# Optimization experiments

Measured on AMD Instinct MI355X. Metric: run time of the kernel, lower is better.

Reference implementation:

```python
import jax, jax.numpy as jnp
import numpy as np

N_X_AXIS = 128
N_Y_AXIS = 128
X_RANGE = (-2.0, 2.0)
Y_RANGE = (-2.0, 2.0)
BATCH = 4
N_CTX = 1024


def make_grid():
    # Give_2d_Grid: flattened (n_x*n_y, 2) grid, x-major (consistent with
    # the view(batch, n_x_axis, n_y_axis, 3) reshape in forward).
    gx = jnp.linspace(X_RANGE[0], X_RANGE[1], N_X_AXIS, dtype=jnp.float32)
    gy = jnp.linspace(Y_RANGE[0], Y_RANGE[1], N_Y_AXIS, dtype=jnp.float32)
    xx, yy = jnp.meshgrid(gx, gy, indexing='ij')  # (n_x, n_y)
    return jnp.stack([xx.ravel(), yy.ravel()], axis=-1)  # (n_x*n_y, 2)


def setup_inputs() -> dict:
    key = jax.random.key(0)
    k1, k2 = jax.random.split(key)
    X = jax.random.normal(k1, (BATCH, N_CTX, 2), dtype=jnp.float32)
    Y = jax.random.normal(k2, (BATCH, N_CTX, 2), dtype=jnp.float32)
    grid = make_grid()
    return {"X": X, "Y": Y, "grid": grid}


def reference(X, Y, grid):
    # RBF Gram matrix between grid points and context points X.
    # k(a,b) = exp(-||a-b||^2 / (2 l^2)), l = 1 (default length scale).
    # d2: (B, G, n)
    d2 = jnp.sum((grid[None, :, None, :] - X[:, None, :, :]) ** 2, axis=-1)
    Gram = jnp.exp(-0.5 * d2)  # (B, G, n)

    # Psi: prepend a column of ones -> (B, n, 3)
    ones = jnp.ones(Y.shape[:2] + (1,), dtype=Y.dtype)
    Expand_Y = jnp.concatenate([ones, Y], axis=-1)

    # Feature map: (B, G, 3)
    FM = jnp.einsum('bgn,bnc->bgc', Gram, Expand_Y)

    # Density-normalize the value channels by the density channel.
    density = FM[..., 0:1]
    FM = jnp.concatenate([density, FM[..., 1:] / density], axis=-1)

    # (B, G, 3) -> (B, n_x, n_y, 3) -> (B, 3, n_y, n_x)
    out = FM.reshape(X.shape[0], N_X_AXIS, N_Y_AXIS, 3)
    return out.transpose(0, 3, 2, 1)
```

## Files before the change

### kernel.cpp

```cpp
#include <hip/hip_runtime.h>


#define N_CTX   1024
#define G_PER_B 16384
#define NQ      64
#define CHUNK   (N_CTX / NQ)
#define TPB     4
#define SSTRIDE (CHUNK + 1)

typedef float fv4 __attribute__((ext_vector_type(4)));

__device__ __forceinline__ float fast_exp2(float x) {
#if __has_builtin(__builtin_amdgcn_exp2f)
  return __builtin_amdgcn_exp2f(x);
#else
  return exp2f(x);
#endif
}

#define RED_BYTES (32 * TPB * 13 * 16)
#define S_BYTES   ((N_CTX + NQ) * 16)

__global__ __launch_bounds__(256, 4) void convcnp_encoder_kernel(
    const float* __restrict__ X,
    const float* __restrict__ Y,
    const float* __restrict__ grid,
    float* __restrict__ out)
{
  __shared__ __attribute__((aligned(16))) unsigned char smem[RED_BYTES];
  float4* s = (float4*)smem;
  fv4 (*red)[TPB][13] = (fv4 (*)[TPB][13])smem;

  const int t    = threadIdx.x;
  const int tile = t & (TPB - 1);
  const int q    = t >> 2;

  const int tau = blockIdx.x * TPB + tile;
  const int b   = tau >> 10;
  const int rem = tau & 1023;
  const int ixt = rem & 31;
  const int jyt = rem >> 5;

  const float SC = 0.84932180028801907f;

  const float2* Xb = (const float2*)(X + b * (N_CTX * 2));
  const float2* Yb = (const float2*)(Y + b * (N_CTX * 2));
#pragma unroll
  for (int k = 0; k < 4; ++k) {
    int n = t + 256 * k;
    float2 x = Xb[n];
    float2 y = Yb[n];
    s[n + (n >> 4)] = make_float4(x.x * SC, x.y * SC, y.x, y.y);
  }

  fv4 gxs;
#pragma unroll
  for (int a = 0; a < 4; ++a)
    gxs[a] = grid[(4 * ixt + a) * 256] * SC;
  float gys[4];
#pragma unroll
  for (int bb = 0; bb < 4; ++bb)
    gys[bb] = grid[2 * (4 * jyt + bb) + 1] * SC;

  __syncthreads();

  fv4 acc0[4], acc1[4], acc2[4];
#pragma unroll
  for (int bb = 0; bb < 4; ++bb) {
    acc0[bb] = (fv4){0.f, 0.f, 0.f, 0.f};
    acc1[bb] = (fv4){0.f, 0.f, 0.f, 0.f};
    acc2[bb] = (fv4){0.f, 0.f, 0.f, 0.f};
  }

  const float4* sp = &s[q * SSTRIDE];
#pragma unroll 4
  for (int it = 0; it < CHUNK; ++it) {
    float4 v = sp[it];
    fv4 dx = gxs - v.x;
    fv4 ex;
#pragma unroll
    for (int a = 0; a < 4; ++a) ex[a] = fast_exp2(-(dx[a] * dx[a]));
    float ey[4], ey0[4], ey1[4];
#pragma unroll
    for (int bb = 0; bb < 4; ++bb) {
      float dy = gys[bb] - v.y;
      float e  = fast_exp2(-(dy * dy));
      ey[bb]  = e;
      ey0[bb] = e * v.z;
      ey1[bb] = e * v.w;
    }
#pragma unroll
    for (int bb = 0; bb < 4; ++bb) {
      acc0[bb] += ex * ey[bb];
      acc1[bb] += ex * ey0[bb];
      acc2[bb] += ex * ey1[bb];
    }
  }

  __syncthreads();

#pragma unroll
  for (int step = 32; step >= 1; step >>= 1) {
    if (q >= step && q < 2 * step) {
      fv4* d = &red[q - step][tile][0];
#pragma unroll
      for (int bb = 0; bb < 4; ++bb) {
        d[bb] = acc0[bb]; d[4 + bb] = acc1[bb]; d[8 + bb] = acc2[bb];
      }
    }
    __syncthreads();
    if (q < step) {
      fv4* r = &red[q][tile][0];
#pragma unroll
      for (int bb = 0; bb < 4; ++bb) {
        acc0[bb] += r[bb]; acc1[bb] += r[4 + bb]; acc2[bb] += r[8 + bb];
      }
    }
    __syncthreads();
  }

  if (q == 0) {
    const int ob = b * (3 * G_PER_B) + jyt * 4 * 128 + ixt * 4;
#pragma unroll
    for (int bb = 0; bb < 4; ++bb) {
      fv4 d  = acc0[bb];
      fv4 o1 = acc1[bb] / d;
      fv4 o2 = acc2[bb] / d;
      const int row = ob + bb * 128;
      *(fv4*)(out + row)                = d;
      *(fv4*)(out + row + G_PER_B)      = o1;
      *(fv4*)(out + row + 2 * G_PER_B)  = o2;
    }
  }
}

extern "C" void kernel_launch(void* const* d_in, const int* in_sizes, int n_in,
                              void* d_out, int out_size, void* d_ws, size_t ws_size,
                              hipStream_t stream) {
  const float* X    = (const float*)d_in[0];
  const float* Y    = (const float*)d_in[1];
  const float* grid = (const float*)d_in[2];
  float* out        = (float*)d_out;

  convcnp_encoder_kernel<<<dim3(1024), dim3(256), 0, stream>>>(X, Y, grid, out);
}
```

Baseline: 71.66 us.

## Factor RBF kernel into separable exp tables and bf16 split-precision MFMA GEMM

Uses the separability of the Gaussian (exp of x-distance times exp of y-distance) to precompute per-axis exponential tables. It stores them as hi/lo bf16 pairs so that three bf16 products recover near-fp32 accuracy. The contraction over context points becomes a split-K MFMA GEMM across many blocks, followed by a finishing kernel that sums the partials and normalises by density. This removes most exp evaluations and the scalar FMA work, at the cost of two extra launches, workspace traffic for tables and partials, and some precision loss from the bf16 split.

After: 77.83 us. +8.6%, slower.

```diff
diff --git a/kernel.cpp b/kernel.cpp
--- a/kernel.cpp
+++ b/kernel.cpp
@@ -1,14 +1,13 @@
 #include <hip/hip_runtime.h>
 
 
-#define N_CTX   1024
-#define G_PER_B 16384
-#define NQ      64
-#define CHUNK   (N_CTX / NQ)
-#define TPB     4
-#define SSTRIDE (CHUNK + 1)
+#define N_CTXP  1024
+#define PL      524288
+#define TABB    (8 * PL * 2)
+#define KSL     24
 
-typedef float fv4 __attribute__((ext_vector_type(4)));
+typedef float  f32x4  __attribute__((ext_vector_type(4)));
+typedef short  bf16x8 __attribute__((ext_vector_type(8)));
 
 __device__ __forceinline__ float fast_exp2(float x) {
 #if __has_builtin(__builtin_amdgcn_exp2f)
@@ -18,120 +17,159 @@
 #endif
 }
 
-#define RED_BYTES (32 * TPB * 13 * 16)
-#define S_BYTES   ((N_CTX + NQ) * 16)
+__device__ __forceinline__ unsigned short f2bf(float v) {
+  unsigned u = __float_as_uint(v);
+  return (unsigned short)((u + 0x7fff + ((u >> 16) & 1)) >> 16);
+}
+__device__ __forceinline__ float bf2f(unsigned short h) {
+  return __uint_as_float(((unsigned)h) << 16);
+}
 
-__global__ __launch_bounds__(256, 4) void convcnp_encoder_kernel(
-    const float* __restrict__ X,
-    const float* __restrict__ Y,
-    const float* __restrict__ grid,
-    float* __restrict__ out)
+__global__ __launch_bounds__(256) void k1_tables(
+    const float* __restrict__ X, const float* __restrict__ Y,
+    const float* __restrict__ grid, unsigned short* __restrict__ tab)
 {
-  __shared__ __attribute__((aligned(16))) unsigned char smem[RED_BYTES];
-  float4* s = (float4*)smem;
-  fv4 (*red)[TPB][13] = (fv4 (*)[TPB][13])smem;
+  const float SC = 0.84932180028801907f;
+  const int tid  = blockIdx.x * 256 + threadIdx.x;
+  const int side = tid >> 16;
+  const int u    = tid & 65535;
+  const int b    = u >> 14;
+  const int i    = (u >> 7) & 127;
+  const int n0   = (u & 127) * 8;
+  const int base = (b * 128 + i) * 1024 + n0;
 
-  const int t    = threadIdx.x;
-  const int tile = t & (TPB - 1);
-  const int q    = t >> 2;
+  const float2* Xb = (const float2*)X + b * 1024 + n0;
+  if (side == 0) {
+    const float gx = grid[i * 256];
+    bf16x8 vh, vl;
+#pragma unroll
+    for (int j = 0; j < 8; ++j) {
+      float d = SC * (gx - Xb[j].x);
+      float e = fast_exp2(-(d * d));
+      unsigned short h = f2bf(e);
+      vh[j] = (short)h;
+      vl[j] = (short)f2bf(e - bf2f(h));
+    }
+    *(bf16x8*)(tab + 0 * PL + base) = vh;
+    *(bf16x8*)(tab + 1 * PL + base) = vl;
+  } else {
+    const float gy = grid[2 * i + 1];
+    const float2* Yb = (const float2*)Y + b * 1024 + n0;
+    bf16x8 eh, el, ah, al, bh, bl;
+#pragma unroll
+    for (int j = 0; j < 8; ++j) {
+      float d  = SC * (gy - Xb[j].y);
+      float e  = fast_exp2(-(d * d));
+      float v0 = e * Yb[j].x;
+      float v1 = e * Yb[j].y;
+      unsigned short h;
+      h = f2bf(e);  eh[j] = (short)h; el[j] = (short)f2bf(e  - bf2f(h));
+      h = f2bf(v0); ah[j] = (short)h; al[j] = (short)f2bf(v0 - bf2f(h));
+      h = f2bf(v1); bh[j] = (short)h; bl[j] = (short)f2bf(v1 - bf2f(h));
+    }
+    *(bf16x8*)(tab + 2 * PL + base) = eh;
+    *(bf16x8*)(tab + 3 * PL + base) = el;
+    *(bf16x8*)(tab + 4 * PL + base) = ah;
+    *(bf16x8*)(tab + 5 * PL + base) = al;
+    *(bf16x8*)(tab + 6 * PL + base) = bh;
+    *(bf16x8*)(tab + 7 * PL + base) = bl;
+  }
+}
 
-  const int tau = blockIdx.x * TPB + tile;
-  const int b   = tau >> 10;
-  const int rem = tau & 1023;
-  const int ixt = rem & 31;
-  const int jyt = rem >> 5;
+__global__ __launch_bounds__(256) void k2_gemm(
+    const unsigned short* __restrict__ tab, float* __restrict__ part)
+{
+  const int bid   = blockIdx.x;
+  const int ks    = bid % KSL;
+  const int r     = bid / KSL;
+  const int ixreg = r & 1, jyreg = (r >> 1) & 1, c = (r >> 2) % 3, b = r / 12;
+  const int sl    = ks >> 3;
+  const int n0    = (ks & 7) * 128;
+  const int Apl   = 2 + 2 * c + (sl == 2 ? 1 : 0);
+  const int Bpl   = (sl == 1) ? 1 : 0;
 
-  const float SC = 0.84932180028801907f;
+  __shared__ unsigned short Alds[64 * 128];
+  __shared__ unsigned short Blds[64 * 128];
 
-  const float2* Xb = (const float2*)(X + b * (N_CTX * 2));
-  const float2* Yb = (const float2*)(Y + b * (N_CTX * 2));
+  const int t = threadIdx.x;
+  const unsigned short* gA = tab + Apl * PL + (b * 128 + jyreg * 64) * 1024 + n0;
+  const unsigned short* gB = tab + Bpl * PL + (b * 128 + ixreg * 64) * 1024 + n0;
+
 #pragma unroll
-  for (int k = 0; k < 4; ++k) {
-    int n = t + 256 * k;
-    float2 x = Xb[n];
-    float2 y = Yb[n];
-    s[n + (n >> 4)] = make_float4(x.x * SC, x.y * SC, y.x, y.y);
+  for (int ch = 0; ch < 4; ++ch) {
+    int flat = ch * 256 + t;
+    int rr = flat >> 4, kc = flat & 15;
+    bf16x8 va = *(const bf16x8*)(gA + rr * 1024 + kc * 8);
+    bf16x8 vb = *(const bf16x8*)(gB + rr * 1024 + kc * 8);
+    int byteoff = (rr * 256 + kc * 16) ^ ((rr & 7) << 4);
+    *(bf16x8*)((char*)Alds + byteoff) = va;
+    *(bf16x8*)((char*)Blds + byteoff) = vb;
+  }
+  __syncthreads();
+
+  const int wid = t >> 6, l = t & 63;
+  const int wr = wid >> 1, wc = wid & 1;
+  const int row16 = l & 15, kg = l >> 4;
+
+  f32x4 acc[2][2] = {};
+#pragma unroll
+  for (int kstep = 0; kstep < 4; ++kstep) {
+    const int kb2 = (kstep * 32 + kg * 8) * 2;
+    bf16x8 a[2], bb[2];
+#pragma unroll
+    for (int tr = 0; tr < 2; ++tr) {
+      int rowA = wr * 32 + tr * 16 + row16;
+      a[tr]  = *(const bf16x8*)((const char*)Alds +
+                ((rowA * 256 + kb2) ^ ((rowA & 7) << 4)));
+      int rowB = wc * 32 + tr * 16 + row16;
+      bb[tr] = *(const bf16x8*)((const char*)Blds +
+                ((rowB * 256 + kb2) ^ ((rowB & 7) << 4)));
+    }
+#pragma unroll
+    for (int tr = 0; tr < 2; ++tr)
+#pragma unroll
+      for (int tc = 0; tc < 2; ++tc)
+        acc[tr][tc] = __builtin_amdgcn_mfma_f32_16x16x32_bf16(
+            a[tr], bb[tc], acc[tr][tc], 0, 0, 0);
   }
 
-  fv4 gxs;
+  float* pt = part + bid * 4096;
 #pragma unroll
-  for (int a = 0; a < 4; ++a)
-    gxs[a] = grid[(4 * ixt + a) * 256] * SC;
-  float gys[4];
+  for (int tr = 0; tr < 2; ++tr)
 #pragma unroll
-  for (int bb = 0; bb < 4; ++bb)
-    gys[bb] = grid[2 * (4 * jyt + bb) + 1] * SC;
+    for (int tc = 0; tc < 2; ++tc)
+#pragma unroll
+      for (int g = 0; g < 4; ++g) {
+        int prow = wr * 32 + tr * 16 + (l >> 4) * 4 + g;
+        int pcol = wc * 32 + tc * 16 + (l & 15);
+        pt[prow * 64 + pcol] = acc[tr][tc][g];
+      }
+}
 
-  __syncthreads();
+__global__ __launch_bounds__(64) void k3_finish(
+    const float* __restrict__ part, float* __restrict__ out)
+{
+  const int tid = blockIdx.x * 64 + threadIdx.x;
+  const int b   = tid >> 12;
+  const int jy  = (tid >> 5) & 127;
+  const int ix0 = (tid & 31) * 4;
+  const int jyreg = jy >> 6, jr = jy & 63;
+  const int ixreg = ix0 >> 6, ir = ix0 & 63;
 
-  fv4 acc0[4], acc1[4], acc2[4];
+  f32x4 s[3];
 #pragma unroll
-  for (int bb = 0; bb < 4; ++bb) {
-    acc0[bb] = (fv4){0.f, 0.f, 0.f, 0.f};
-    acc1[bb] = (fv4){0.f, 0.f, 0.f, 0.f};
-    acc2[bb] = (fv4){0.f, 0.f, 0.f, 0.f};
+  for (int c = 0; c < 3; ++c) {
+    const int bid0 = (b * 12 + c * 4 + jyreg * 2 + ixreg) * KSL;
+    f32x4 acc = {};
+#pragma unroll
+    for (int k = 0; k < KSL; ++k)
+      acc += *(const f32x4*)(part + (bid0 + k) * 4096 + jr * 64 + ir);
+    s[c] = acc;
   }
-
-  const float4* sp = &s[q * SSTRIDE];
-#pragma unroll 4
-  for (int it = 0; it < CHUNK; ++it) {
-    float4 v = sp[it];
-    fv4 dx = gxs - v.x;
-    fv4 ex;
-#pragma unroll
-    for (int a = 0; a < 4; ++a) ex[a] = fast_exp2(-(dx[a] * dx[a]));
-    float ey[4], ey0[4], ey1[4];
-#pragma unroll
-    for (int bb = 0; bb < 4; ++bb) {
-      float dy = gys[bb] - v.y;
-      float e  = fast_exp2(-(dy * dy));
-      ey[bb]  = e;
-      ey0[bb] = e * v.z;
-      ey1[bb] = e * v.w;
-    }
-#pragma unroll
-    for (int bb = 0; bb < 4; ++bb) {
-      acc0[bb] += ex * ey[bb];
-      acc1[bb] += ex * ey0[bb];
-      acc2[bb] += ex * ey1[bb];
-    }
-  }
-
-  __syncthreads();
-
-#pragma unroll
-  for (int step = 32; step >= 1; step >>= 1) {
-    if (q >= step && q < 2 * step) {
-      fv4* d = &red[q - step][tile][0];
-#pragma unroll
-      for (int bb = 0; bb < 4; ++bb) {
-        d[bb] = acc0[bb]; d[4 + bb] = acc1[bb]; d[8 + bb] = acc2[bb];
-      }
-    }
-    __syncthreads();
-    if (q < step) {
-      fv4* r = &red[q][tile][0];
-#pragma unroll
-      for (int bb = 0; bb < 4; ++bb) {
-        acc0[bb] += r[bb]; acc1[bb] += r[4 + bb]; acc2[bb] += r[8 + bb];
-      }
-    }
-    __syncthreads();
-  }
-
-  if (q == 0) {
-    const int ob = b * (3 * G_PER_B) + jyt * 4 * 128 + ixt * 4;
-#pragma unroll
-    for (int bb = 0; bb < 4; ++bb) {
-      fv4 d  = acc0[bb];
-      fv4 o1 = acc1[bb] / d;
-      fv4 o2 = acc2[bb] / d;
-      const int row = ob + bb * 128;
-      *(fv4*)(out + row)                = d;
-      *(fv4*)(out + row + G_PER_B)      = o1;
-      *(fv4*)(out + row + 2 * G_PER_B)  = o2;
-    }
-  }
+  const int ob = ((b * 3 + 0) * 128 + jy) * 128 + ix0;
+  *(f32x4*)(out + ob)         = s[0];
+  *(f32x4*)(out + ob + 16384) = s[1] / s[0];
+  *(f32x4*)(out + ob + 32768) = s[2] / s[0];
 }
 
 extern "C" void kernel_launch(void* const* d_in, const int* in_sizes, int n_in,
@@ -142,5 +180,10 @@
   const float* grid = (const float*)d_in[2];
   float* out        = (float*)d_out;
 
-  convcnp_encoder_kernel<<<dim3(1024), dim3(256), 0, stream>>>(X, Y, grid, out);
+  unsigned short* tab = (unsigned short*)d_ws;
+  float* part = (float*)((char*)d_ws + TABB);
+
+  k1_tables<<<dim3(512),  dim3(256), 0, stream>>>(X, Y, grid, tab);
+  k2_gemm  <<<dim3(1152), dim3(256), 0, stream>>>(tab, part);
+  k3_finish<<<dim3(256),  dim3(64),  0, stream>>>(part, out);
 }
```

## Recast separable RBF accumulation as fp16 MFMA matmul over context panels

Applied to the files above, without the earlier changes.

The kernel now uses the fact that the RBF kernel separates into an x factor and a y factor. Each block builds fp16 panels of exp(y) terms, weighted by Y values, and of exp(x) terms in swizzled shared memory. It then contracts them over context points with 16x16x32 MFMA instructions. This replaces the per-thread scalar outer-product accumulation and the shared-memory tree reduction, and cuts exp evaluations from O(G·n) to O((nx+ny)·n). The cost is fp16 precision in the Gram factors and products, and a grid of only 64 blocks of 512 threads, which may underfill the GPU.

Result: faster. 65.25 us (-8.9%).

```diff
diff --git a/kernel.cpp b/kernel.cpp
--- a/kernel.cpp
+++ b/kernel.cpp
@@ -1,14 +1,10 @@
 #include <hip/hip_runtime.h>
 
 
-#define N_CTX   1024
-#define G_PER_B 16384
-#define NQ      64
-#define CHUNK   (N_CTX / NQ)
-#define TPB     4
-#define SSTRIDE (CHUNK + 1)
+#define NCTX 1024
 
-typedef float fv4 __attribute__((ext_vector_type(4)));
+typedef float    f32x4 __attribute__((ext_vector_type(4)));
+typedef _Float16 f16x8 __attribute__((ext_vector_type(8)));
 
 __device__ __forceinline__ float fast_exp2(float x) {
 #if __has_builtin(__builtin_amdgcn_exp2f)
@@ -18,118 +14,107 @@
 #endif
 }
 
-#define RED_BYTES (32 * TPB * 13 * 16)
-#define S_BYTES   ((N_CTX + NQ) * 16)
-
-__global__ __launch_bounds__(256, 4) void convcnp_encoder_kernel(
+__global__ __launch_bounds__(512) void convcnp_fused_kernel(
     const float* __restrict__ X,
     const float* __restrict__ Y,
     const float* __restrict__ grid,
     float* __restrict__ out)
 {
-  __shared__ __attribute__((aligned(16))) unsigned char smem[RED_BYTES];
-  float4* s = (float4*)smem;
-  fv4 (*red)[TPB][13] = (fv4 (*)[TPB][13])smem;
+  __shared__ float4 xy[NCTX];
+  __shared__ unsigned char panel[4 * 8192];
+  __shared__ f32x4 den[4][64];
 
-  const int t    = threadIdx.x;
-  const int tile = t & (TPB - 1);
-  const int q    = t >> 2;
-
-  const int tau = blockIdx.x * TPB + tile;
-  const int b   = tau >> 10;
-  const int rem = tau & 1023;
-  const int ixt = rem & 31;
-  const int jyt = rem >> 5;
+  const int t = threadIdx.x;
+  const int w = t >> 6, l = t & 63;
+  const int bid = blockIdx.x;
+  const int b = bid >> 4, jyt = (bid >> 2) & 3, ixt = bid & 3;
 
   const float SC = 0.84932180028801907f;
 
-  const float2* Xb = (const float2*)(X + b * (N_CTX * 2));
-  const float2* Yb = (const float2*)(Y + b * (N_CTX * 2));
+  const float2* Xb = (const float2*)X + b * NCTX;
+  const float2* Yb = (const float2*)Y + b * NCTX;
 #pragma unroll
-  for (int k = 0; k < 4; ++k) {
-    int n = t + 256 * k;
+  for (int k = 0; k < 2; ++k) {
+    int n = t + 512 * k;
     float2 x = Xb[n];
     float2 y = Yb[n];
-    s[n + (n >> 4)] = make_float4(x.x * SC, x.y * SC, y.x, y.y);
+    xy[n] = make_float4(x.x * SC, x.y * SC, y.x, y.y);
   }
 
-  fv4 gxs;
-#pragma unroll
-  for (int a = 0; a < 4; ++a)
-    gxs[a] = grid[(4 * ixt + a) * 256] * SC;
-  float gys[4];
-#pragma unroll
-  for (int bb = 0; bb < 4; ++bb)
-    gys[bb] = grid[2 * (4 * jyt + bb) + 1] * SC;
+  const int r  = t & 31;
+  const int g8 = t >> 5;
+  const float gxs = grid[(ixt * 32 + r) * 256] * SC;
+  const float gys = grid[2 * (jyt * 32 + r) + 1] * SC;
+  const int wbase = ((r * 256 + g8 * 16) ^ ((r & 15) << 4));
+
+  const int trc = w & 3, tr = trc >> 1, tc = trc & 1;
+  const int cA = (w < 4) ? 0 : 1;
+  const int row16 = l & 15, kg = l >> 4;
+  const int arow = tr * 16 + row16, brow = tc * 16 + row16;
+  const int aswz = (arow & 15) << 4, bswz = (brow & 15) << 4;
+
+  f32x4 accA = {0.f, 0.f, 0.f, 0.f};
+  f32x4 accB = {0.f, 0.f, 0.f, 0.f};
 
   __syncthreads();
 
-  fv4 acc0[4], acc1[4], acc2[4];
+  for (int q = 0; q < 8; ++q) {
+    const int n0 = q * 128 + g8 * 8;
+    f16x8 ve, v0, v1, vx;
 #pragma unroll
-  for (int bb = 0; bb < 4; ++bb) {
-    acc0[bb] = (fv4){0.f, 0.f, 0.f, 0.f};
-    acc1[bb] = (fv4){0.f, 0.f, 0.f, 0.f};
-    acc2[bb] = (fv4){0.f, 0.f, 0.f, 0.f};
-  }
+    for (int j = 0; j < 8; ++j) {
+      float4 v = xy[n0 + j];
+      float dx = gxs - v.x;
+      float ex = fast_exp2(-(dx * dx));
+      float dy = gys - v.y;
+      float ey = fast_exp2(-(dy * dy));
+      ve[j] = (_Float16)ey;
+      v0[j] = (_Float16)(ey * v.z);
+      v1[j] = (_Float16)(ey * v.w);
+      vx[j] = (_Float16)ex;
+    }
+    *(f16x8*)(panel + 0 * 8192 + wbase) = ve;
+    *(f16x8*)(panel + 1 * 8192 + wbase) = v0;
+    *(f16x8*)(panel + 2 * 8192 + wbase) = v1;
+    *(f16x8*)(panel + 3 * 8192 + wbase) = vx;
+    __syncthreads();
 
-  const float4* sp = &s[q * SSTRIDE];
-#pragma unroll 4
-  for (int it = 0; it < CHUNK; ++it) {
-    float4 v = sp[it];
-    fv4 dx = gxs - v.x;
-    fv4 ex;
+    const unsigned char* Ap = panel + cA * 8192;
+    const unsigned char* A2 = panel + 2 * 8192;
+    const unsigned char* Bp = panel + 3 * 8192;
 #pragma unroll
-    for (int a = 0; a < 4; ++a) ex[a] = fast_exp2(-(dx[a] * dx[a]));
-    float ey[4], ey0[4], ey1[4];
-#pragma unroll
-    for (int bb = 0; bb < 4; ++bb) {
-      float dy = gys[bb] - v.y;
-      float e  = fast_exp2(-(dy * dy));
-      ey[bb]  = e;
-      ey0[bb] = e * v.z;
-      ey1[bb] = e * v.w;
-    }
-#pragma unroll
-    for (int bb = 0; bb < 4; ++bb) {
-      acc0[bb] += ex * ey[bb];
-      acc1[bb] += ex * ey0[bb];
-      acc2[bb] += ex * ey1[bb];
-    }
-  }
-
-  __syncthreads();
-
-#pragma unroll
-  for (int step = 32; step >= 1; step >>= 1) {
-    if (q >= step && q < 2 * step) {
-      fv4* d = &red[q - step][tile][0];
-#pragma unroll
-      for (int bb = 0; bb < 4; ++bb) {
-        d[bb] = acc0[bb]; d[4 + bb] = acc1[bb]; d[8 + bb] = acc2[bb];
-      }
-    }
-    __syncthreads();
-    if (q < step) {
-      fv4* r = &red[q][tile][0];
-#pragma unroll
-      for (int bb = 0; bb < 4; ++bb) {
-        acc0[bb] += r[bb]; acc1[bb] += r[4 + bb]; acc2[bb] += r[8 + bb];
+    for (int kk = 0; kk < 4; ++kk) {
+      const int kb = kk * 64 + kg * 16;
+      f16x8 af = *(const f16x8*)(Ap + ((arow * 256 + kb) ^ aswz));
+      f16x8 bf = *(const f16x8*)(Bp + ((brow * 256 + kb) ^ bswz));
+      accA = __builtin_amdgcn_mfma_f32_16x16x32_f16(af, bf, accA, 0, 0, 0);
+      if (w < 4) {
+        f16x8 a2 = *(const f16x8*)(A2 + ((arow * 256 + kb) ^ aswz));
+        accB = __builtin_amdgcn_mfma_f32_16x16x32_f16(a2, bf, accB, 0, 0, 0);
       }
     }
     __syncthreads();
   }
 
-  if (q == 0) {
-    const int ob = b * (3 * G_PER_B) + jyt * 4 * 128 + ixt * 4;
+  const int jy0 = jyt * 32 + tr * 16 + kg * 4;
+  const int ix  = ixt * 32 + tc * 16 + row16;
+  float* ob = out + b * 3 * 16384;
+  if (w < 4) {
+    den[w][l] = accA;
 #pragma unroll
-    for (int bb = 0; bb < 4; ++bb) {
-      fv4 d  = acc0[bb];
-      fv4 o1 = acc1[bb] / d;
-      fv4 o2 = acc2[bb] / d;
-      const int row = ob + bb * 128;
-      *(fv4*)(out + row)                = d;
-      *(fv4*)(out + row + G_PER_B)      = o1;
-      *(fv4*)(out + row + 2 * G_PER_B)  = o2;
+    for (int g = 0; g < 4; ++g) {
+      const int o = (jy0 + g) * 128 + ix;
+      ob[o]             = accA[g];
+      ob[2 * 16384 + o] = accB[g] / accA[g];
+    }
+  }
+  __syncthreads();
+  if (w >= 4) {
+    f32x4 d = den[w - 4][l];
+#pragma unroll
+    for (int g = 0; g < 4; ++g) {
+      const int o = (jy0 + g) * 128 + ix;
+      ob[1 * 16384 + o] = accA[g] / d[g];
     }
   }
 }
@@ -142,5 +127,5 @@
   const float* grid = (const float*)d_in[2];
   float* out        = (float*)d_out;
 
-  convcnp_encoder_kernel<<<dim3(1024), dim3(256), 0, stream>>>(X, Y, grid, out);
+  convcnp_fused_kernel<<<dim3(64), dim3(512), 0, stream>>>(X, Y, grid, out);
 }
```
